# Optimization experiments

Hardware: AMD Instinct MI355X
Metric: run time of the kernel (lower is better)

## Reference

```python
import jax, jax.numpy as jnp
import numpy as np

B, S, D, H = 32, 2048, 128, 16  # batch, cached kv len, head dim (=d_model), heads
EPS = 1e-5


def setup_inputs() -> dict:
    key = jax.random.key(0)
    ks = jax.random.split(key, 5)
    d_total = D * H
    x = jax.random.normal(ks[0], (B, 1, D), jnp.float32)
    past_k = jax.random.normal(ks[1], (B, H, S, D), jnp.float32)
    past_v = jax.random.normal(ks[2], (B, H, S, D), jnp.float32)
    Wqkv = jax.random.normal(ks[3], (3 * d_total, D), jnp.float32) * 0.02
    bqkv = jnp.zeros((3 * d_total,), jnp.float32)
    Wout = jax.random.normal(ks[4], (D, d_total), jnp.float32) * 0.02
    bout = jnp.zeros((D,), jnp.float32)
    return {"x": x, "past_k": past_k, "past_v": past_v,
            "Wqkv": Wqkv, "bqkv": bqkv, "Wout": Wout, "bout": bout}


def reference(x, past_k, past_v, Wqkv, bqkv, Wout, bout):
    # QKV projection: (B,1,D) -> (B,1,3*H*D)
    qkv = x @ Wqkv.T + bqkv
    qkv = qkv.reshape(B, 1, 3 * H, D).transpose(0, 2, 1, 3)  # (B,3H,1,D)
    q, k_new, v_new = jnp.split(qkv, 3, axis=1)              # each (B,H,1,D)
    k = jnp.concatenate([past_k, k_new], axis=2)             # (B,H,S+1,D)
    v = jnp.concatenate([past_v, v_new], axis=2)
    # single-query attention (causal mask is trivially all-visible for q_len=1)
    scale = 1.0 / jnp.sqrt(jnp.float32(D))
    scores = jnp.einsum('bhqd,bhkd->bhqk', q, k) * scale     # (B,H,1,S+1)
    probs = jax.nn.softmax(scores, axis=-1)
    y = jnp.einsum('bhqk,bhkd->bhqd', probs, v)              # (B,H,1,D)
    y = y.transpose(0, 2, 1, 3).reshape(B, 1, H * D)         # (B,1,H*D)
    y = y @ Wout.T + bout                                    # (B,1,D)
    y = y + x                                                # residual
    # layer norm over last dim, no affine params
    mu = jnp.mean(y, axis=-1, keepdims=True)
    var = jnp.mean(jnp.square(y - mu), axis=-1, keepdims=True)
    out = (y - mu) / jnp.sqrt(var + EPS)
    return (out, k, v)
```

## Files before the change

kernel.cpp:

```cpp
#include <hip/hip_runtime.h>
#include <math.h>

#define B 32
#define S 2048
#define S1 2049
#define D 128
#define H 16
#define DT 2048
#define EPS 1e-5f
#define SCALE 0.08838834764831845f

typedef float f4v __attribute__((ext_vector_type(4)));

__global__ void __launch_bounds__(1024)
attn_kernel(const float* __restrict__ x,
            const float* __restrict__ Wqkv,
            const float* __restrict__ bqkv,
            const float* __restrict__ past_k,
            const float* __restrict__ past_v,
            float* __restrict__ out_k,
            float* __restrict__ out_v,
            float* __restrict__ ys_g) {
    const int bh = blockIdx.x;
    const int b = bh >> 4;
    const int h = bh & (H - 1);
    const int tid  = threadIdx.x;
    const int wave = tid >> 6;
    const int lane = tid & 63;
    const int l32  = tid & 31;
    const int rg   = tid >> 5;

    __shared__ float xs[D];
    __shared__ float qkvs[3 * D];
    __shared__ float sc[S1 + 3];
    __shared__ float swm[16];
    __shared__ float swl[16];
    __shared__ float sacc[32 * D];

    const f4v* __restrict__ kin  = (const f4v*)past_k + (size_t)bh * S * 32;
    const f4v* __restrict__ vin  = (const f4v*)past_v + (size_t)bh * S * 32;
    f4v* __restrict__ kout = (f4v*)out_k + (size_t)bh * S1 * 32;
    f4v* __restrict__ vout = (f4v*)out_v + (size_t)bh * S1 * 32;

    if (tid < D) xs[tid] = x[b * D + tid];
    __syncthreads();
    if (tid < 3 * D) {
        const int which = tid >> 7;
        const int d = tid & 127;
        const int row = which * DT + h * D + d;
        const float* w = Wqkv + (size_t)row * D;
        float acc = bqkv[row];
#pragma unroll
        for (int j = 0; j < D; j += 4) {
            float4 w4 = *reinterpret_cast<const float4*>(w + j);
            acc = fmaf(w4.x, xs[j + 0], acc);
            acc = fmaf(w4.y, xs[j + 1], acc);
            acc = fmaf(w4.z, xs[j + 2], acc);
            acc = fmaf(w4.w, xs[j + 3], acc);
        }
        qkvs[tid] = acc;
        if (which == 1) ((float*)kout)[(size_t)S * D + d] = acc;
        if (which == 2) ((float*)vout)[(size_t)S * D + d] = acc;
    }
    __syncthreads();

    const f4v q4 = ((const f4v*)qkvs)[l32];

#pragma unroll 8
    for (int it = 0; it < S / 32; ++it) {
        const int r = it * 32 + rg;
        const size_t off = (size_t)r * 32 + l32;
        f4v k4 = __builtin_nontemporal_load(&kin[off]);
        kout[off] = k4;
        f4v t = k4 * q4;
        float p = t.x + t.y + t.z + t.w;
        p += __shfl_xor(p, 1);
        p += __shfl_xor(p, 2);
        p += __shfl_xor(p, 4);
        p += __shfl_xor(p, 8);
        p += __shfl_xor(p, 16);
        if (l32 == 0) sc[r] = p * SCALE;
    }
    if (tid < 64) {
        float pd = qkvs[2 * tid] * qkvs[D + 2 * tid]
                 + qkvs[2 * tid + 1] * qkvs[D + 2 * tid + 1];
        pd += __shfl_xor(pd, 1);
        pd += __shfl_xor(pd, 2);
        pd += __shfl_xor(pd, 4);
        pd += __shfl_xor(pd, 8);
        pd += __shfl_xor(pd, 16);
        pd += __shfl_xor(pd, 32);
        if (tid == 0) sc[S] = pd * SCALE;
    }
    __syncthreads();

    const float s0v = sc[tid];
    const float s1v = sc[tid + 1024];
    const float sxv = (tid == 0) ? sc[S] : -1e30f;
    float m = fmaxf(fmaxf(s0v, s1v), sxv);
#pragma unroll
    for (int off = 1; off < 64; off <<= 1) m = fmaxf(m, __shfl_xor(m, off));
    if (lane == 0) swm[wave] = m;
    __syncthreads();
    float M = swm[0];
#pragma unroll
    for (int g = 1; g < 16; ++g) M = fmaxf(M, swm[g]);
    const float e0 = __expf(s0v - M);
    const float e1 = __expf(s1v - M);
    sc[tid] = e0;
    sc[tid + 1024] = e1;
    float lsum = e0 + e1;
    if (tid == 0) {
        const float e2 = __expf(sxv - M);
        sc[S] = e2;
        lsum += e2;
    }
#pragma unroll
    for (int off = 1; off < 64; off <<= 1) lsum += __shfl_xor(lsum, off);
    if (lane == 0) swl[wave] = lsum;
    __syncthreads();
    float L = swl[0];
#pragma unroll
    for (int g = 1; g < 16; ++g) L += swl[g];
    const float invL = 1.0f / L;

    f4v acc = (f4v){0.f, 0.f, 0.f, 0.f};
#pragma unroll 8
    for (int it = 0; it < S / 32; ++it) {
        const int r = it * 32 + rg;
        const size_t off = (size_t)r * 32 + l32;
        f4v v4 = __builtin_nontemporal_load(&vin[off]);
        vout[off] = v4;
        acc += v4 * sc[r];
    }

    ((f4v*)sacc)[rg * 32 + l32] = acc;
    __syncthreads();

    if (tid < D) {
        float y = 0.f;
#pragma unroll
        for (int g = 0; g < 32; ++g) y += sacc[g * D + tid];
        y = fmaf(sc[S], qkvs[2 * D + tid], y);
        ys_g[(size_t)bh * D + tid] = y * invL;
    }
}

__global__ void __launch_bounds__(1024)
out_proj_kernel(const float* __restrict__ x,
                const float* __restrict__ ys_g,
                const float* __restrict__ Wout,
                const float* __restrict__ bout,
                float* __restrict__ out) {
    const int b = blockIdx.x;
    const int t = threadIdx.x;
    __shared__ float ys[DT];
    __shared__ float pp[D * 8];
    __shared__ float tb[D];

    ys[t]        = ys_g[(size_t)b * DT + t];
    ys[t + 1024] = ys_g[(size_t)b * DT + t + 1024];
    __syncthreads();

    {
        const int d = t >> 3;
        const int sub = t & 7;
        const float* w = Wout + (size_t)d * DT + sub * 256;
        const float* y = ys + sub * 256;
        float acc = 0.f;
#pragma unroll
        for (int j = 0; j < 256; j += 4) {
            float4 w4 = *reinterpret_cast<const float4*>(w + j);
            acc = fmaf(w4.x, y[j + 0], acc);
            acc = fmaf(w4.y, y[j + 1], acc);
            acc = fmaf(w4.z, y[j + 2], acc);
            acc = fmaf(w4.w, y[j + 3], acc);
        }
        pp[d * 8 + sub] = acc;
    }
    __syncthreads();

    float val = 0.f;
    if (t < D) {
        float a = 0.f;
#pragma unroll
        for (int g = 0; g < 8; ++g) a += pp[t * 8 + g];
        val = a + bout[t] + x[b * D + t];
        tb[t] = val;
    }
    __syncthreads();
    for (int off = 64; off > 0; off >>= 1) {
        if (t < off) tb[t] += tb[t + off];
        __syncthreads();
    }
    const float mu = tb[0] * (1.0f / D);
    __syncthreads();
    const float diff = val - mu;
    if (t < D) tb[t] = diff * diff;
    __syncthreads();
    for (int off = 64; off > 0; off >>= 1) {
        if (t < off) tb[t] += tb[t + off];
        __syncthreads();
    }
    const float var = tb[0] * (1.0f / D);
    if (t < D) out[(size_t)b * D + t] = diff / sqrtf(var + EPS);
}

extern "C" void kernel_launch(void* const* d_in, const int* in_sizes, int n_in,
                              void* d_out, int out_size, void* d_ws, size_t ws_size,
                              hipStream_t stream) {
    const float* x      = (const float*)d_in[0];
    const float* past_k = (const float*)d_in[1];
    const float* past_v = (const float*)d_in[2];
    const float* Wqkv   = (const float*)d_in[3];
    const float* bqkv   = (const float*)d_in[4];
    const float* Wout   = (const float*)d_in[5];
    const float* bout   = (const float*)d_in[6];

    float* out   = (float*)d_out;
    float* out_k = out + (size_t)B * D;
    float* out_v = out_k + (size_t)B * H * S1 * D;

    float* ys_g = (float*)d_ws;

    attn_kernel<<<B * H, 1024, 0, stream>>>(
        x, Wqkv, bqkv, past_k, past_v, out_k, out_v, ys_g);
    out_proj_kernel<<<B, 1024, 0, stream>>>(
        x, ys_g, Wout, bout, out);
}
```

Measured before the change: 441.3 us.

## Fuse output projection into attention kernel via last-block counter; use DPP reductions

Merges the output projection and layer norm into the attention kernel. Each batch's last-finishing head block, found through an atomic counter, does the projection and normalisation, so the second kernel launch goes away. A small reset kernel zeroes the counters before each launch. The score reduction switches from five shuffles to four DPP row adds, with two half-row partial buffers summed later. The extra shared memory may lower occupancy, and the fused tail now runs serially in the last block of each batch.

```diff
diff --git a/kernel.cpp b/kernel.cpp
--- a/kernel.cpp
+++ b/kernel.cpp
@@ -12,15 +12,36 @@
 
 typedef float f4v __attribute__((ext_vector_type(4)));
 
+__device__ __forceinline__ float dpp_row_sum16(float x) {
+    int xi;
+    xi = __builtin_amdgcn_update_dpp(0, __float_as_int(x), 0x121, 0xf, 0xf, false);
+    x += __int_as_float(xi);
+    xi = __builtin_amdgcn_update_dpp(0, __float_as_int(x), 0x122, 0xf, 0xf, false);
+    x += __int_as_float(xi);
+    xi = __builtin_amdgcn_update_dpp(0, __float_as_int(x), 0x124, 0xf, 0xf, false);
+    x += __int_as_float(xi);
+    xi = __builtin_amdgcn_update_dpp(0, __float_as_int(x), 0x128, 0xf, 0xf, false);
+    x += __int_as_float(xi);
+    return x;
+}
+
+__global__ void reset_kernel(unsigned* __restrict__ c) {
+    if (threadIdx.x < B) c[threadIdx.x] = 0u;
+}
+
 __global__ void __launch_bounds__(1024)
 attn_kernel(const float* __restrict__ x,
             const float* __restrict__ Wqkv,
             const float* __restrict__ bqkv,
             const float* __restrict__ past_k,
             const float* __restrict__ past_v,
+            const float* __restrict__ Wout,
+            const float* __restrict__ bout,
             float* __restrict__ out_k,
             float* __restrict__ out_v,
-            float* __restrict__ ys_g) {
+            float* __restrict__ ys_g,
+            unsigned* __restrict__ counters,
+            float* __restrict__ out) {
     const int bh = blockIdx.x;
     const int b = bh >> 4;
     const int h = bh & (H - 1);
@@ -32,10 +53,16 @@
 
     __shared__ float xs[D];
     __shared__ float qkvs[3 * D];
-    __shared__ float sc[S1 + 3];
+    __shared__ float scp[2 * S];
     __shared__ float swm[16];
     __shared__ float swl[16];
     __shared__ float sacc[32 * D];
+    __shared__ float sh_snew;
+    __shared__ float sh_enew;
+    __shared__ unsigned sh_last;
+    __shared__ float ys[DT];
+    __shared__ float pp[D * 8];
+    __shared__ float tb[D];
 
     const f4v* __restrict__ kin  = (const f4v*)past_k + (size_t)bh * S * 32;
     const f4v* __restrict__ vin  = (const f4v*)past_v + (size_t)bh * S * 32;
@@ -64,23 +91,6 @@
     }
     __syncthreads();
 
-    const f4v q4 = ((const f4v*)qkvs)[l32];
-
-#pragma unroll 8
-    for (int it = 0; it < S / 32; ++it) {
-        const int r = it * 32 + rg;
-        const size_t off = (size_t)r * 32 + l32;
-        f4v k4 = __builtin_nontemporal_load(&kin[off]);
-        kout[off] = k4;
-        f4v t = k4 * q4;
-        float p = t.x + t.y + t.z + t.w;
-        p += __shfl_xor(p, 1);
-        p += __shfl_xor(p, 2);
-        p += __shfl_xor(p, 4);
-        p += __shfl_xor(p, 8);
-        p += __shfl_xor(p, 16);
-        if (l32 == 0) sc[r] = p * SCALE;
-    }
     if (tid < 64) {
         float pd = qkvs[2 * tid] * qkvs[D + 2 * tid]
                  + qkvs[2 * tid + 1] * qkvs[D + 2 * tid + 1];
@@ -90,13 +100,27 @@
         pd += __shfl_xor(pd, 8);
         pd += __shfl_xor(pd, 16);
         pd += __shfl_xor(pd, 32);
-        if (tid == 0) sc[S] = pd * SCALE;
-    }
-    __syncthreads();
-
-    const float s0v = sc[tid];
-    const float s1v = sc[tid + 1024];
-    const float sxv = (tid == 0) ? sc[S] : -1e30f;
+        if (tid == 0) sh_snew = pd * SCALE;
+    }
+
+    const f4v q4 = ((const f4v*)qkvs)[l32];
+
+#pragma unroll 8
+    for (int it = 0; it < S / 32; ++it) {
+        const int r = it * 32 + rg;
+        const size_t off = (size_t)r * 32 + l32;
+        f4v k4 = __builtin_nontemporal_load(&kin[off]);
+        kout[off] = k4;
+        f4v t = k4 * q4;
+        float p = t.x + t.y + t.z + t.w;
+        p = dpp_row_sum16(p);
+        if ((l32 & 15) == 0) scp[(l32 >> 4) * S + r] = p * SCALE;
+    }
+    __syncthreads();
+
+    const float s0v = scp[tid] + scp[S + tid];
+    const float s1v = scp[tid + 1024] + scp[S + tid + 1024];
+    const float sxv = (tid == 0) ? sh_snew : -1e30f;
     float m = fmaxf(fmaxf(s0v, s1v), sxv);
 #pragma unroll
     for (int off = 1; off < 64; off <<= 1) m = fmaxf(m, __shfl_xor(m, off));
@@ -107,13 +131,12 @@
     for (int g = 1; g < 16; ++g) M = fmaxf(M, swm[g]);
     const float e0 = __expf(s0v - M);
     const float e1 = __expf(s1v - M);
-    sc[tid] = e0;
-    sc[tid + 1024] = e1;
+    scp[tid] = e0;
+    scp[tid + 1024] = e1;
     float lsum = e0 + e1;
     if (tid == 0) {
-        const float e2 = __expf(sxv - M);
-        sc[S] = e2;
-        lsum += e2;
+        sh_enew = __expf(sh_snew - M);
+        lsum += sh_enew;
     }
 #pragma unroll
     for (int off = 1; off < 64; off <<= 1) lsum += __shfl_xor(lsum, off);
@@ -131,7 +154,7 @@
         const size_t off = (size_t)r * 32 + l32;
         f4v v4 = __builtin_nontemporal_load(&vin[off]);
         vout[off] = v4;
-        acc += v4 * sc[r];
+        acc += v4 * scp[r];
     }
 
     ((f4v*)sacc)[rg * 32 + l32] = acc;
@@ -141,69 +164,63 @@
         float y = 0.f;
 #pragma unroll
         for (int g = 0; g < 32; ++g) y += sacc[g * D + tid];
-        y = fmaf(sc[S], qkvs[2 * D + tid], y);
+        y = fmaf(sh_enew, qkvs[2 * D + tid], y);
         ys_g[(size_t)bh * D + tid] = y * invL;
     }
-}
-
-__global__ void __launch_bounds__(1024)
-out_proj_kernel(const float* __restrict__ x,
-                const float* __restrict__ ys_g,
-                const float* __restrict__ Wout,
-                const float* __restrict__ bout,
-                float* __restrict__ out) {
-    const int b = blockIdx.x;
-    const int t = threadIdx.x;
-    __shared__ float ys[DT];
-    __shared__ float pp[D * 8];
-    __shared__ float tb[D];
-
-    ys[t]        = ys_g[(size_t)b * DT + t];
-    ys[t + 1024] = ys_g[(size_t)b * DT + t + 1024];
+    __threadfence();
+    __syncthreads();
+    if (tid == 0)
+        sh_last = (atomicAdd(&counters[b], 1u) == H - 1) ? 1u : 0u;
+    __syncthreads();
+    if (!sh_last) return;
+
+    __threadfence();
+    ys[tid]        = ys_g[(size_t)b * DT + tid];
+    ys[tid + 1024] = ys_g[(size_t)b * DT + tid + 1024];
     __syncthreads();
 
     {
-        const int d = t >> 3;
-        const int sub = t & 7;
+        const int d = tid >> 3;
+        const int sub = tid & 7;
         const float* w = Wout + (size_t)d * DT + sub * 256;
         const float* y = ys + sub * 256;
-        float acc = 0.f;
+        float a = 0.f;
 #pragma unroll
         for (int j = 0; j < 256; j += 4) {
             float4 w4 = *reinterpret_cast<const float4*>(w + j);
-            acc = fmaf(w4.x, y[j + 0], acc);
-            acc = fmaf(w4.y, y[j + 1], acc);
-            acc = fmaf(w4.z, y[j + 2], acc);
-            acc = fmaf(w4.w, y[j + 3], acc);
+            a = fmaf(w4.x, y[j + 0], a);
+            a = fmaf(w4.y, y[j + 1], a);
+            a = fmaf(w4.z, y[j + 2], a);
+            a = fmaf(w4.w, y[j + 3], a);
         }
-        pp[d * 8 + sub] = acc;
+        pp[d * 8 + sub] = a;
     }
     __syncthreads();
 
     float val = 0.f;
-    if (t < D) {
+    if (tid < D) {
         float a = 0.f;
 #pragma unroll
-        for (int g = 0; g < 8; ++g) a += pp[t * 8 + g];
-        val = a + bout[t] + x[b * D + t];
-        tb[t] = val;
+        for (int g = 0; g < 8; ++g) a += pp[tid * 8 + g];
+        val = a + bout[tid] + xs[tid];
+        tb[tid] = val;
     }
     __syncthreads();
     for (int off = 64; off > 0; off >>= 1) {
-        if (t < off) tb[t] += tb[t + off];
+        if (tid < off) tb[tid] += tb[tid + off];
         __syncthreads();
     }
     const float mu = tb[0] * (1.0f / D);
     __syncthreads();
     const float diff = val - mu;
-    if (t < D) tb[t] = diff * diff;
+    if (tid < D) tb[tid] = diff * diff;
     __syncthreads();
     for (int off = 64; off > 0; off >>= 1) {
-        if (t < off) tb[t] += tb[t + off];
+        if (tid < off) tb[tid] += tb[tid + off];
         __syncthreads();
     }
     const float var = tb[0] * (1.0f / D);
-    if (t < D) out[(size_t)b * D + t] = diff / sqrtf(var + EPS);
+    if (tid < D) out[(size_t)b * D + tid] = diff / sqrtf(var + EPS);
 }
 
 extern "C" void kernel_launch(void* const* d_in, const int* in_sizes, int n_in,
@@ -221,10 +238,11 @@
     float* out_k = out + (size_t)B * D;
     float* out_v = out_k + (size_t)B * H * S1 * D;
 
-    float* ys_g = (float*)d_ws;
-
+    float*    ys_g     = (float*)d_ws;
+    unsigned* counters = (unsigned*)(ys_g + (size_t)B * DT);
+
+    reset_kernel<<<1, 64, 0, stream>>>(counters);
     attn_kernel<<<B * H, 1024, 0, stream>>>(
-        x, Wqkv, bqkv, past_k, past_v, out_k, out_v, ys_g);
-    out_proj_kernel<<<B, 1024, 0, stream>>>(
-        x, ys_g, Wout, bout, out);
-}
+        x, Wqkv, bqkv, past_k, past_v, Wout, bout,
+        out_k, out_v, ys_g, counters, out);
+}
```

Result: slower. 833.7 us (+88.9%).
